# Performance work log

Hardware: AMD Instinct MI355X
Metric: run time of the kernel (lower is better)

The kernel has to match this reference:

```python
import jax, jax.numpy as jnp
import numpy as np

D_MODEL = 1024
N_HEADS = 16
D_HEAD = D_MODEL // N_HEADS


def setup_inputs() -> dict:
    key = jax.random.key(0)
    kx, kq, kk, kv, ko = jax.random.split(key, 5)
    s = 1.0 / np.sqrt(D_MODEL)
    return {
        "x": jax.random.normal(kx, (2, 2048, D_MODEL), dtype=jnp.float32),
        "Wq": jax.random.normal(kq, (D_MODEL, D_MODEL), dtype=jnp.float32) * s,
        "Wk": jax.random.normal(kk, (D_MODEL, D_MODEL), dtype=jnp.float32) * s,
        "Wv": jax.random.normal(kv, (D_MODEL, D_MODEL), dtype=jnp.float32) * s,
        "Wo": jax.random.normal(ko, (D_MODEL, D_MODEL), dtype=jnp.float32) * s,
    }


def reference(x, Wq, Wk, Wv, Wo):
    B, T, _ = x.shape
    def split_heads(t):  # [B,T,D] -> [B,H,T,d]
        return t.reshape(B, T, N_HEADS, D_HEAD).transpose(0, 2, 1, 3)
    q = split_heads(x @ Wq)
    k = split_heads(x @ Wk)
    v = split_heads(x @ Wv)
    scale = jnp.asarray(D_HEAD, x.dtype) ** -0.5
    att = jnp.einsum("bhqd,bhkd->bhqk", q, k) * scale
    mask = jnp.tril(jnp.ones((T, T), dtype=x.dtype))  # 1 on/below diag
    att = att + (1.0 - mask)[None, None] * jnp.asarray(-1e9, x.dtype)
    w = jax.nn.softmax(att, axis=-1)
    y = jnp.einsum("bhqk,bhkd->bhqd", w, v)
    y = y.transpose(0, 2, 1, 3).reshape(B, T, D_MODEL)
    return y @ Wo
```

## Files before the change

### kernel.cpp

```cpp
#include <hip/hip_runtime.h>

#define DM 1024
#define NH 16
#define TT 2048
#define BB 2
#define NTOK (BB*TT)
#define DQKV 3072

typedef __attribute__((ext_vector_type(8))) short bf16x8;
typedef __attribute__((ext_vector_type(4))) float f32x4;
typedef __attribute__((ext_vector_type(4))) int  int4v;

static __device__ __forceinline__ short f2b(float f) {
  union { float f; unsigned u; } v; v.f = f;
  unsigned r = v.u + 0x7FFFu + ((v.u >> 16) & 1u);
  return (short)(r >> 16);
}

__global__ __launch_bounds__(256) void k_convert(const float* __restrict__ in,
                                                 short* __restrict__ out, int n) {
  int i = (blockIdx.x * 256 + threadIdx.x) * 8;
  if (i >= n) return;
  float4 a = *(const float4*)(in + i);
  float4 b = *(const float4*)(in + i + 4);
  bf16x8 o;
  o[0]=f2b(a.x); o[1]=f2b(a.y); o[2]=f2b(a.z); o[3]=f2b(a.w);
  o[4]=f2b(b.x); o[5]=f2b(b.y); o[6]=f2b(b.z); o[7]=f2b(b.w);
  *(bf16x8*)(out + i) = o;
}

__global__ __launch_bounds__(256) void k_transpose_w4(const float* __restrict__ Wq,
                                                      const float* __restrict__ Wk,
                                                      const float* __restrict__ Wv,
                                                      const float* __restrict__ Wo,
                                                      short* __restrict__ WqkvT,
                                                      short* __restrict__ WoT) {
  __shared__ short t[64][72];
  const int z = blockIdx.z;
  const float* W = (z == 0) ? Wq : (z == 1) ? Wk : (z == 2) ? Wv : Wo;
  short* Wt = (z < 3) ? WqkvT : WoT;
  const int row0 = (z < 3) ? z * 1024 : 0;
  int tid = threadIdx.x;
  int n0 = blockIdx.x * 64, k0 = blockIdx.y * 64;
  #pragma unroll
  for (int i = 0; i < 4; i++) {
    int id = tid + 256 * i;
    int r = id >> 4;
    int c = id & 15;
    float4 v = *(const float4*)(W + (size_t)(k0 + r) * DM + n0 + c * 4);
    t[c*4+0][r] = f2b(v.x);
    t[c*4+1][r] = f2b(v.y);
    t[c*4+2][r] = f2b(v.z);
    t[c*4+3][r] = f2b(v.w);
  }
  __syncthreads();
  #pragma unroll
  for (int i = 0; i < 2; i++) {
    int id = tid + 256 * i;
    int r = id >> 3;
    int c = id & 7;
    bf16x8 o = *(const bf16x8*)&t[r][c * 8];
    *(bf16x8*)(Wt + (size_t)(row0 + n0 + r) * DM + k0 + c * 8) = o;
  }
}

__global__ __launch_bounds__(256) void k_transpose_v(const short* __restrict__ V,
                                                     short* __restrict__ Vt) {
  __shared__ short t[64][72];
  int tid = threadIdx.x;
  int bh = blockIdx.y;
  int b = bh >> 4, h = bh & 15;
  int t0 = blockIdx.x * 64;
  #pragma unroll
  for (int i = 0; i < 2; i++) {
    int id = tid + 256 * i;
    int r = id >> 3;
    int c = id & 7;
    bf16x8 v = *(const bf16x8*)(V + (size_t)(b * TT + t0 + r) * DQKV + h * 64 + c * 8);
    #pragma unroll
    for (int e = 0; e < 8; e++) t[c * 8 + e][r] = v[e];
  }
  __syncthreads();
  #pragma unroll
  for (int i = 0; i < 2; i++) {
    int id = tid + 256 * i;
    int r = id >> 3;
    int c = id & 7;
    bf16x8 o = *(const bf16x8*)&t[r][c * 8];
    *(bf16x8*)(Vt + (size_t)(bh * 64 + r) * TT + t0 + c * 8) = o;
  }
}

template<int OUT_BF16, int BN>
__global__ __launch_bounds__(256) void k_gemm_lds(const short* __restrict__ A,
                                                  const short* __restrict__ Bt,
                                                  void* __restrict__ C,
                                                  int M, int N, int K,
                                                  int qcols, float qscale) {
  __shared__ short As[2][128 * 64];
  __shared__ short Bs[2][BN * 64];
  constexpr int NI = BN / 32;
  const int tid = threadIdx.x;
  const int lane = tid & 63, w = tid >> 6;
  const int wm = w >> 1, wn = w & 1;
  const int l15 = lane & 15, g = lane >> 4;
  const int nx = N / BN;
  const int cx = nx >> 3;
  const int bid = blockIdx.x;
  const int xcd = bid & 7, k_ = bid >> 3;
  const int bx = xcd * cx + (k_ % cx), by = k_ / cx;
  const int m0 = by * 128, n0 = bx * BN;
  const int srow = lane >> 3;
  const int scol = ((lane & 7) ^ srow) * 8;
  const int rsw = l15 & 7;

  auto stage = [&](int buf, int k0) {
    #pragma unroll
    for (int i = 0; i < 4; i++) {
      int rbase = w * 32 + i * 8;
      __builtin_amdgcn_global_load_lds(
        (const __attribute__((address_space(1))) void*)(A + (size_t)(m0 + rbase + srow) * K + k0 + scol),
        (__attribute__((address_space(3))) void*)&As[buf][rbase * 64],
        16, 0, 0);
    }
    #pragma unroll
    for (int i = 0; i < BN / 32; i++) {
      int rbase = w * (BN / 4) + i * 8;
      __builtin_amdgcn_global_load_lds(
        (const __attribute__((address_space(1))) void*)(Bt + (size_t)(n0 + rbase + srow) * K + k0 + scol),
        (__attribute__((address_space(3))) void*)&Bs[buf][rbase * 64],
        16, 0, 0);
    }
  };

  f32x4 acc[4][NI] = {};
  stage(0, 0);
  __syncthreads();
  const int nt = K / 64;
  for (int t = 0; t < nt; t++) {
    const int cur = t & 1;
    if (t + 1 < nt) stage(cur ^ 1, (t + 1) * 64);
    #pragma unroll
    for (int kk = 0; kk < 64; kk += 32) {
      bf16x8 af[4], bfr[NI];
      #pragma unroll
      for (int mi = 0; mi < 4; mi++)
        af[mi] = *(const bf16x8*)&As[cur][(wm * 64 + mi * 16 + l15) * 64 + ((((kk >> 3) + g) ^ rsw) << 3)];
      #pragma unroll
      for (int ni = 0; ni < NI; ni++)
        bfr[ni] = *(const bf16x8*)&Bs[cur][(wn * (BN / 2) + ni * 16 + l15) * 64 + ((((kk >> 3) + g) ^ rsw) << 3)];
      #pragma unroll
      for (int mi = 0; mi < 4; mi++)
        #pragma unroll
        for (int ni = 0; ni < NI; ni++)
          acc[mi][ni] = __builtin_amdgcn_mfma_f32_16x16x32_bf16(af[mi], bfr[ni], acc[mi][ni], 0, 0, 0);
    }
    __syncthreads();
  }
  #pragma unroll
  for (int mi = 0; mi < 4; mi++) {
    #pragma unroll
    for (int ni = 0; ni < NI; ni++) {
      #pragma unroll
      for (int j = 0; j < 4; j++) {
        int row = m0 + wm * 64 + mi * 16 + g * 4 + j;
        int col = n0 + wn * (BN / 2) + ni * 16 + l15;
        float v = acc[mi][ni][j];
        if (OUT_BF16) {
          if (col < qcols) v *= qscale;
          ((short*)C)[(size_t)row * N + col] = f2b(v);
        } else {
          ((float*)C)[(size_t)row * N + col] = v;
        }
      }
    }
  }
}

__global__ __launch_bounds__(256) void k_attn(const short* __restrict__ Qkv,
                                              const short* __restrict__ Vt,
                                              short* __restrict__ Y) {
  __shared__ short Ks[2][64 * 64];
  __shared__ short Vs[2][64 * 64];
  __shared__ short Ps[4][16 * 64];
  const int tid = threadIdx.x;
  const int lane = tid & 63, w = tid >> 6;
  const int l15 = lane & 15, g = lane >> 4;
  const int bx = blockIdx.x;
  const int xcd = bx & 7, idx = bx >> 3;
  const int bh = xcd * 4 + (idx & 3);
  const int qt = 31 - (idx >> 2);
  const int b = bh >> 4, h = bh & 15;
  const int q0 = qt * 64;
  const int nkt = qt + 1;
  const short* Qb = Qkv;
  const short* Kb = Qkv + DM;
  short* PsW = Ps[w];
  const int rsw = l15 & 7;

  auto stage = [&](int buf, int kt) {
    #pragma unroll
    for (int i = 0; i < 2; i++) {
      int id = tid + 256 * i;
      int r = id >> 3;
      int cl = (id ^ r) & 7;
      __builtin_amdgcn_global_load_lds(
        (const __attribute__((address_space(1))) void*)(Kb + (size_t)(b * TT + kt * 64 + r) * DQKV + h * 64 + cl * 8),
        (__attribute__((address_space(3))) void*)&Ks[buf][(w * 64 + 256 * i) * 8],
        16, 0, 0);
      __builtin_amdgcn_global_load_lds(
        (const __attribute__((address_space(1))) void*)(Vt + (size_t)(bh * 64 + r) * TT + kt * 64 + cl * 8),
        (__attribute__((address_space(3))) void*)&Vs[buf][(w * 64 + 256 * i) * 8],
        16, 0, 0);
    }
  };

  bf16x8 aq[2];
  #pragma unroll
  for (int kc = 0; kc < 2; kc++)
    aq[kc] = *(const bf16x8*)(Qb + (size_t)(b * TT + q0 + w * 16 + l15) * DQKV + h * 64 + kc * 32 + 8 * g);

  f32x4 accO[4] = {};
  float m2[4], lp[4];
  #pragma unroll
  for (int j = 0; j < 4; j++) { m2[j] = -1e30f; lp[j] = 0.f; }

  stage(0, 0);
  __syncthreads();

  for (int kt = 0; kt < nkt; kt++) {
    const int cur = kt & 1;
    if (kt + 1 < nkt) stage(cur ^ 1, kt + 1);

    f32x4 accS[4] = {};
    __builtin_amdgcn_s_setprio(1);
    #pragma unroll
    for (int n = 0; n < 4; n++) {
      #pragma unroll
      for (int kc = 0; kc < 2; kc++) {
        bf16x8 bk = *(const bf16x8*)&Ks[cur][(n * 16 + l15) * 64 + (((kc * 4 + g) ^ rsw) << 3)];
        accS[n] = __builtin_amdgcn_mfma_f32_16x16x32_bf16(aq[kc], bk, accS[n], 0, 0, 0);
      }
    }
    __builtin_amdgcn_s_setprio(0);

    float tmaxp[4];
    #pragma unroll
    for (int j = 0; j < 4; j++) tmaxp[j] = -1e30f;
    const int qbase = q0 + w * 16 + g * 4;
    if (kt == qt) {
      #pragma unroll
      for (int n = 0; n < 4; n++) {
        int key = kt * 64 + n * 16 + l15;
        #pragma unroll
        for (int j = 0; j < 4; j++) {
          float s = accS[n][j];
          if (key > qbase + j) s = -1e30f;
          accS[n][j] = s;
          tmaxp[j] = fmaxf(tmaxp[j], s);
        }
      }
    } else {
      #pragma unroll
      for (int n = 0; n < 4; n++)
        #pragma unroll
        for (int j = 0; j < 4; j++)
          tmaxp[j] = fmaxf(tmaxp[j], accS[n][j]);
    }

    float dmax = fmaxf(fmaxf(tmaxp[0] - m2[0], tmaxp[1] - m2[1]),
                       fmaxf(tmaxp[2] - m2[2], tmaxp[3] - m2[3]));
    if (!__all(dmax <= 8.0f)) {
      #pragma unroll
      for (int j = 0; j < 4; j++) {
        float t = tmaxp[j];
        #pragma unroll
        for (int off = 1; off < 16; off <<= 1)
          t = fmaxf(t, __shfl_xor(t, off));
        float mnew = fmaxf(m2[j], t);
        float al = exp2f(m2[j] - mnew);
        m2[j] = mnew;
        lp[j] *= al;
        #pragma unroll
        for (int n2 = 0; n2 < 4; n2++) accO[n2][j] *= al;
      }
    }

    #pragma unroll
    for (int n = 0; n < 4; n++) {
      #pragma unroll
      for (int j = 0; j < 4; j++) {
        float e = exp2f(accS[n][j] - m2[j]);
        lp[j] += e;
        union { float f; unsigned u; } cv; cv.f = e;
        int row = g * 4 + j;
        int cl = 2 * n + (l15 >> 3);
        PsW[row * 64 + (((cl ^ (row & 7))) << 3) + (l15 & 7)] = (short)(cv.u >> 16);
      }
    }

    __builtin_amdgcn_s_setprio(1);
    #pragma unroll
    for (int kc = 0; kc < 2; kc++) {
      bf16x8 pa = *(const bf16x8*)&PsW[l15 * 64 + (((kc * 4 + g) ^ rsw) << 3)];
      #pragma unroll
      for (int n2 = 0; n2 < 4; n2++) {
        bf16x8 vb = *(const bf16x8*)&Vs[cur][(n2 * 16 + l15) * 64 + (((kc * 4 + g) ^ rsw) << 3)];
        accO[n2] = __builtin_amdgcn_mfma_f32_16x16x32_bf16(pa, vb, accO[n2], 0, 0, 0);
      }
    }
    __builtin_amdgcn_s_setprio(0);

    __syncthreads();
  }

  float lr[4];
  #pragma unroll
  for (int j = 0; j < 4; j++) {
    float s = lp[j];
    #pragma unroll
    for (int off = 1; off < 16; off <<= 1)
      s += __shfl_xor(s, off);
    lr[j] = s;
  }
  const int orow = b * TT + q0 + w * 16;
  #pragma unroll
  for (int n2 = 0; n2 < 4; n2++) {
    #pragma unroll
    for (int j = 0; j < 4; j++) {
      float v = accO[n2][j] / lr[j];
      Y[(size_t)(orow + g * 4 + j) * DM + h * 64 + n2 * 16 + l15] = f2b(v);
    }
  }
}

extern "C" void kernel_launch(void* const* d_in, const int* in_sizes, int n_in,
                              void* d_out, int out_size, void* d_ws, size_t ws_size,
                              hipStream_t stream) {
  const float* x  = (const float*)d_in[0];
  const float* Wq = (const float*)d_in[1];
  const float* Wk = (const float*)d_in[2];
  const float* Wv = (const float*)d_in[3];
  const float* Wo = (const float*)d_in[4];
  float* out = (float*)d_out;

  char* ws = (char*)d_ws;
  size_t off = 0;
  auto alloc = [&](size_t bytes) {
    char* p = ws + off;
    off += (bytes + 255) & ~(size_t)255;
    return p;
  };
  short* xb    = (short*)alloc((size_t)NTOK * DM * 2);
  short* WqkvT = (short*)alloc((size_t)DQKV * DM * 2);
  short* WoT   = (short*)alloc((size_t)DM * DM * 2);
  short* Qkv   = (short*)alloc((size_t)NTOK * DQKV * 2);
  short* Vt    = (short*)alloc((size_t)NTOK * DM * 2);
  short* Yb    = xb;
  if (off > ws_size) return;

  k_convert<<<(NTOK * DM) / (256 * 8), 256, 0, stream>>>(x, xb, NTOK * DM);
  k_transpose_w4<<<dim3(DM / 64, DM / 64, 4), 256, 0, stream>>>(Wq, Wk, Wv, Wo, WqkvT, WoT);

  const float QSC = 0.125f * 1.44269504088896f;
  k_gemm_lds<1, 128><<<dim3((DQKV / 128) * (NTOK / 128)), 256, 0, stream>>>(xb, WqkvT, Qkv, NTOK, DQKV, DM, DM, QSC);

  k_transpose_v<<<dim3(TT / 64, BB * NH), 256, 0, stream>>>(Qkv + 2048, Vt);
  k_attn<<<dim3(1024), 256, 0, stream>>>(Qkv, Vt, Yb);

  k_gemm_lds<0, 64><<<dim3((DM / 64) * (NTOK / 128)), 256, 0, stream>>>(Yb, WoT, out, NTOK, DM, DM, 0, 1.0f);
}
```

Before: 118.8 us.

## Use partial vmcnt waits to keep next-tile prefetch in flight across barriers

Replaces __syncthreads in the GEMM and attention loops with explicit s_waitcnt vmcnt(N) plus raw s_barrier. The wait is issued after the next tile's global_load_lds prefetch, so only the current tile's loads must land and the prefetch stays outstanding during compute. This removes the full vmcnt(0) drain that __syncthreads implies. It relies on hand-counted load instruction numbers per stage, which could break correctness if the compiler splits or reorders loads.

Result: slower. 122.7 us (+3.3%).

```diff
diff --git a/kernel.cpp b/kernel.cpp
--- a/kernel.cpp
+++ b/kernel.cpp
@@ -100,6 +100,7 @@
   __shared__ short As[2][128 * 64];
   __shared__ short Bs[2][BN * 64];
   constexpr int NI = BN / 32;
+  constexpr int NLOADS = 4 + BN / 32;
   const int tid = threadIdx.x;
   const int lane = tid & 63, w = tid >> 6;
   const int wm = w >> 1, wn = w & 1;
@@ -135,11 +136,19 @@
 
   f32x4 acc[4][NI] = {};
   stage(0, 0);
-  __syncthreads();
   const int nt = K / 64;
   for (int t = 0; t < nt; t++) {
     const int cur = t & 1;
-    if (t + 1 < nt) stage(cur ^ 1, (t + 1) * 64);
+    if (t + 1 < nt) {
+      stage(cur ^ 1, (t + 1) * 64);
+      if constexpr (NLOADS == 8) asm volatile("s_waitcnt vmcnt(8)" ::: "memory");
+      else                       asm volatile("s_waitcnt vmcnt(6)" ::: "memory");
+    } else {
+      asm volatile("s_waitcnt vmcnt(0)" ::: "memory");
+    }
+    __builtin_amdgcn_sched_barrier(0);
+    __builtin_amdgcn_s_barrier();
+    __builtin_amdgcn_sched_barrier(0);
     #pragma unroll
     for (int kk = 0; kk < 64; kk += 32) {
       bf16x8 af[4], bfr[NI];
@@ -155,7 +164,8 @@
         for (int ni = 0; ni < NI; ni++)
           acc[mi][ni] = __builtin_amdgcn_mfma_f32_16x16x32_bf16(af[mi], bfr[ni], acc[mi][ni], 0, 0, 0);
     }
-    __syncthreads();
+    __builtin_amdgcn_sched_barrier(0);
+    __builtin_amdgcn_s_barrier();
   }
   #pragma unroll
   for (int mi = 0; mi < 4; mi++) {
@@ -226,11 +236,18 @@
   for (int j = 0; j < 4; j++) { m2[j] = -1e30f; lp[j] = 0.f; }
 
   stage(0, 0);
-  __syncthreads();
 
   for (int kt = 0; kt < nkt; kt++) {
     const int cur = kt & 1;
-    if (kt + 1 < nkt) stage(cur ^ 1, kt + 1);
+    if (kt + 1 < nkt) {
+      stage(cur ^ 1, kt + 1);
+      asm volatile("s_waitcnt vmcnt(4)" ::: "memory");
+    } else {
+      asm volatile("s_waitcnt vmcnt(0)" ::: "memory");
+    }
+    __builtin_amdgcn_sched_barrier(0);
+    __builtin_amdgcn_s_barrier();
+    __builtin_amdgcn_sched_barrier(0);
 
     f32x4 accS[4] = {};
     __builtin_amdgcn_s_setprio(1);
@@ -311,7 +328,8 @@
     }
     __builtin_amdgcn_s_setprio(0);
 
-    __syncthreads();
+    __builtin_amdgcn_sched_barrier(0);
+    __builtin_amdgcn_s_barrier();
   }
 
   float lr[4];
```

## Pack P stores, permute V key order, compute row sums via MFMA

Applied to the files above, without the earlier changes.

The attention kernel now writes the probability tile to LDS as packed 4-value (8-byte) stores instead of scalar 2-byte stores. The keys are permuted so that each lane's four score columns become contiguous, and the V transpose applies the matching permutation to the key axis. The softmax denominator is now built by an extra MFMA of P against a vector of ones, which replaces the per-element scalar adds and the final shuffle reduction. This costs one extra MFMA per k-chunk and uses bf16-rounded P in the denominator, which now matches the numerator exactly.

After: 115.4 us. 2.8% less time.

```diff
diff --git a/kernel.cpp b/kernel.cpp
--- a/kernel.cpp
+++ b/kernel.cpp
@@ -76,9 +76,10 @@
     int id = tid + 256 * i;
     int r = id >> 3;
     int c = id & 7;
+    int kp = ((r & 15) << 2) | (r >> 4);
     bf16x8 v = *(const bf16x8*)(V + (size_t)(b * TT + t0 + r) * DQKV + h * 64 + c * 8);
     #pragma unroll
-    for (int e = 0; e < 8; e++) t[c * 8 + e][r] = v[e];
+    for (int e = 0; e < 8; e++) t[c * 8 + e][kp] = v[e];
   }
   __syncthreads();
   #pragma unroll
@@ -198,6 +199,8 @@
   short* PsW = Ps[w];
   const int rsw = l15 & 7;
 
+  const bf16x8 vones = {0x3F80, 0x3F80, 0x3F80, 0x3F80, 0x3F80, 0x3F80, 0x3F80, 0x3F80};
+
   auto stage = [&](int buf, int kt) {
     #pragma unroll
     for (int i = 0; i < 2; i++) {
@@ -221,9 +224,10 @@
     aq[kc] = *(const bf16x8*)(Qb + (size_t)(b * TT + q0 + w * 16 + l15) * DQKV + h * 64 + kc * 32 + 8 * g);
 
   f32x4 accO[4] = {};
-  float m2[4], lp[4];
-  #pragma unroll
-  for (int j = 0; j < 4; j++) { m2[j] = -1e30f; lp[j] = 0.f; }
+  f32x4 accL = {};
+  float m2[4];
+  #pragma unroll
+  for (int j = 0; j < 4; j++) m2[j] = -1e30f;
 
   stage(0, 0);
   __syncthreads();
@@ -280,23 +284,25 @@
         float mnew = fmaxf(m2[j], t);
         float al = exp2f(m2[j] - mnew);
         m2[j] = mnew;
-        lp[j] *= al;
+        accL[j] *= al;
         #pragma unroll
         for (int n2 = 0; n2 < 4; n2++) accO[n2][j] *= al;
       }
     }
 
     #pragma unroll
-    for (int n = 0; n < 4; n++) {
-      #pragma unroll
-      for (int j = 0; j < 4; j++) {
-        float e = exp2f(accS[n][j] - m2[j]);
-        lp[j] += e;
-        union { float f; unsigned u; } cv; cv.f = e;
-        int row = g * 4 + j;
-        int cl = 2 * n + (l15 >> 3);
-        PsW[row * 64 + (((cl ^ (row & 7))) << 3) + (l15 & 7)] = (short)(cv.u >> 16);
-      }
+    for (int j = 0; j < 4; j++) {
+      const int row = g * 4 + j;
+      union { float f; unsigned u; } c0, c1, c2, c3;
+      c0.f = exp2f(accS[0][j] - m2[j]);
+      c1.f = exp2f(accS[1][j] - m2[j]);
+      c2.f = exp2f(accS[2][j] - m2[j]);
+      c3.f = exp2f(accS[3][j] - m2[j]);
+      int2 pk;
+      pk.x = (int)((c0.u >> 16) | (c1.u & 0xFFFF0000u));
+      pk.y = (int)((c2.u >> 16) | (c3.u & 0xFFFF0000u));
+      const int c8 = l15 ^ ((row & 7) << 1);
+      *(int2*)&PsW[row * 64 + (c8 << 2)] = pk;
     }
 
     __builtin_amdgcn_s_setprio(1);
@@ -308,27 +314,22 @@
         bf16x8 vb = *(const bf16x8*)&Vs[cur][(n2 * 16 + l15) * 64 + (((kc * 4 + g) ^ rsw) << 3)];
         accO[n2] = __builtin_amdgcn_mfma_f32_16x16x32_bf16(pa, vb, accO[n2], 0, 0, 0);
       }
+      accL = __builtin_amdgcn_mfma_f32_16x16x32_bf16(pa, vones, accL, 0, 0, 0);
     }
     __builtin_amdgcn_s_setprio(0);
 
     __syncthreads();
   }
 
-  float lr[4];
-  #pragma unroll
-  for (int j = 0; j < 4; j++) {
-    float s = lp[j];
-    #pragma unroll
-    for (int off = 1; off < 16; off <<= 1)
-      s += __shfl_xor(s, off);
-    lr[j] = s;
-  }
+  float inv[4];
+  #pragma unroll
+  for (int j = 0; j < 4; j++) inv[j] = 1.0f / accL[j];
   const int orow = b * TT + q0 + w * 16;
   #pragma unroll
   for (int n2 = 0; n2 < 4; n2++) {
     #pragma unroll
     for (int j = 0; j < 4; j++) {
-      float v = accO[n2][j] / lr[j];
+      float v = accO[n2][j] * inv[j];
       Y[(size_t)(orow + g * 4 + j) * DM + h * 64 + n2 * 16 + l15] = f2b(v);
     }
   }
```
